# Optimization experiments

Measured on AMD Instinct MI355X. Metric: run time of the kernel, lower is better.

The kernel has to match this reference:

```python
import jax, jax.numpy as jnp
import numpy as np

E = 8        # numExperts
D = 1024     # d_model
F = 4096     # expert hidden = 4*d_model
T = 8192     # total tokens (sum of expertFrequency)


def setup_inputs() -> dict:
    key = jax.random.key(0)
    k0, k1, k2, k3, k4 = jax.random.split(key, 5)
    expertOrderedInput = jax.random.normal(k0, (T, D), dtype=jnp.float32)
    # Static equal split so the split sizes are jit-compatible.
    expertFrequency = jnp.full((E,), T // E, dtype=jnp.int64)
    s1 = 1.0 / np.sqrt(D)
    s2 = 1.0 / np.sqrt(F)
    w1 = jax.random.normal(k1, (E, D, F), dtype=jnp.float32) * s1
    b1 = jnp.zeros((E, F), dtype=jnp.float32)
    w2 = jax.random.normal(k2, (E, F, D), dtype=jnp.float32) * s2
    b2 = jnp.zeros((E, D), dtype=jnp.float32)
    return {"expertOrderedInput": expertOrderedInput,
            "expertFrequency": expertFrequency,
            "w1": w1, "b1": b1, "w2": w2, "b2": b2}


def reference(expertOrderedInput, expertFrequency, w1, b1, w2, b2):
    # expertOrderedInput: [T, D], tokens pre-sorted by expert.
    # expertFrequency is equal per expert (T/E each), so the
    # split-loop-cat in the torch module is exactly a grouped GEMM.
    e = w1.shape[0]
    t = expertOrderedInput.shape[0]
    x = expertOrderedInput.reshape(e, t // e, -1)            # [E, T/E, D]
    h = jax.nn.gelu(jnp.einsum('etd,edf->etf', x, w1) + b1[:, None, :])
    y = jnp.einsum('etf,efd->etd', h, w2) + b2[:, None, :]   # [E, T/E, D]
    return y.reshape(t, -1)                                   # cat along dim 0
```

## Files before the change

kernel.cpp:

```cpp
#include <hip/hip_runtime.h>

#define E_ 8
#define D_ 1024
#define F_ 4096
#define T_ 8192

typedef unsigned short u16;
typedef short bf16x8 __attribute__((ext_vector_type(8)));
typedef float f32x4 __attribute__((ext_vector_type(4)));
typedef unsigned short u16x8 __attribute__((ext_vector_type(8)));

__device__ __forceinline__ u16 f2bf(float f) {
    unsigned u = __builtin_bit_cast(unsigned, f);
    u += 0x7fffu + ((u >> 16) & 1u);
    return (u16)(u >> 16);
}

__device__ __forceinline__ float gelu_tanh(float x) {
    const float k0 = 0.7978845608028654f;
    const float k1 = 0.044715f;
    float t = tanhf(k0 * (x + k1 * x * x * x));
    return 0.5f * x * (1.0f + t);
}

__device__ __forceinline__ void async16(const void* g, void* l) {
    __builtin_amdgcn_global_load_lds(
        (const __attribute__((address_space(1))) unsigned int*)g,
        (__attribute__((address_space(3))) unsigned int*)l, 16, 0, 0);
}

__global__ void cvt_x(const float* __restrict__ in, u16* __restrict__ out) {
    int i = blockIdx.x * 256 + threadIdx.x;
    const float4* in4 = (const float4*)in;
    float4 a = in4[2 * i], b = in4[2 * i + 1];
    u16x8 o;
    o[0] = f2bf(a.x); o[1] = f2bf(a.y); o[2] = f2bf(a.z); o[3] = f2bf(a.w);
    o[4] = f2bf(b.x); o[5] = f2bf(b.y); o[6] = f2bf(b.z); o[7] = f2bf(b.w);
    *(u16x8*)(out + (size_t)i * 8) = o;
}

__global__ void transpose_cvt(const float* __restrict__ src, u16* __restrict__ dst,
                              int R, int C) {
    __shared__ float tile[32][33];
    int e = blockIdx.z;
    src += (size_t)e * R * C;
    dst += (size_t)e * R * C;
    int c0 = blockIdx.x * 32, r0 = blockIdx.y * 32;
    int tx = threadIdx.x, ty = threadIdx.y;
#pragma unroll
    for (int i = 0; i < 4; ++i)
        tile[ty + i * 8][tx] = src[(size_t)(r0 + ty + i * 8) * C + c0 + tx];
    __syncthreads();
#pragma unroll
    for (int i = 0; i < 4; ++i)
        dst[(size_t)(c0 + ty + i * 8) * R + r0 + tx] = f2bf(tile[tx][ty + i * 8]);
}

template <int BN, int WM, int WN, int EPI, int NM, int NN>
__global__ __launch_bounds__(512, 2) void gemm8p(
    const u16* __restrict__ A,
    const u16* __restrict__ Bt,
    const float* __restrict__ bias,
    void* __restrict__ Cv,
    int Mpe, int N, int K) {
    constexpr int BM  = 256;
    constexpr int LA  = 2;
    constexpr int LB  = BN / 128;
    constexpr int WTM = BM / WM;
    constexpr int MFR = WTM / 16;
    constexpr int AELEM = 4 * BM * 32;
    constexpr int VMC = 2 * (LA + LB);
    __shared__ u16 lds[AELEM + 4 * BN * 32];

    const int tid = threadIdx.x;
    const int w = tid >> 6, lane = tid & 63;
    const int lr = lane & 15, lg = lane >> 4;
    const int wm = w / WN, wn = w % WN;

    constexpr int NWG = E_ * NM * NN;
    constexpr int PER = NWG / 8;
    const int bid = blockIdx.x;
    const int logical = (bid & 7) * PER + (bid >> 3);
    const int e   = logical / (NM * NN);
    const int rem = logical % (NM * NN);
    const int bn  = rem / NM;
    const int bm  = rem % NM;

    A    += (size_t)e * Mpe * K;
    Bt   += (size_t)e * N * K;
    bias += (size_t)e * N;
    const int n0 = bn * BN;
    const int m0 = bm * BM;
    const int NT = K >> 6;

    const char* gA[LA];
    const char* gB[LB];
    {
        int kch = (lane & 3) ^ ((lane >> 3) & 3);
#pragma unroll
        for (int i = 0; i < LA; ++i) {
            int row = i * 128 + w * 16 + (lane >> 2);
            gA[i] = (const char*)(A + (size_t)(m0 + row) * K + kch * 8);
        }
#pragma unroll
        for (int i = 0; i < LB; ++i) {
            int row = i * 128 + w * 16 + (lane >> 2);
            gB[i] = (const char*)(Bt + (size_t)(n0 + row) * K + kch * 8);
        }
    }
    char* ldsc = (char*)lds;

    auto stageA = [&](int t, int h) {
        size_t goff = (size_t)t * 128 + (size_t)h * 64;
        unsigned dst = (unsigned)((((t & 1) * 2 + h) * (BM * 64)) + w * 1024);
#pragma unroll
        for (int i = 0; i < LA; ++i)
            async16(gA[i] + goff, ldsc + dst + i * 8192);
    };
    auto stageB = [&](int t, int h) {
        size_t goff = (size_t)t * 128 + (size_t)h * 64;
        unsigned dst = (unsigned)(AELEM * 2 + (((t & 1) * 2 + h) * (BN * 64)) + w * 1024);
#pragma unroll
        for (int i = 0; i < LB; ++i)
            async16(gB[i] + goff, ldsc + dst + i * 8192);
    };

    f32x4 acc[MFR][4];
    const f32x4 zero = {0.f, 0.f, 0.f, 0.f};
#pragma unroll
    for (int i = 0; i < MFR; ++i)
#pragma unroll
        for (int j = 0; j < 4; ++j) acc[i][j] = zero;

    stageA(0, 0); stageB(0, 0); stageA(0, 1); stageB(0, 1);
    stageA(1, 0); stageB(1, 0);
    asm volatile("s_waitcnt vmcnt(%0)" :: "i"(VMC) : "memory");
    __builtin_amdgcn_s_barrier();
    __builtin_amdgcn_sched_barrier(0);

    const u16* SBbase = lds + AELEM;
    bf16x8 a[MFR];
    const int arow = wm * WTM + lr;
    const int brow = wn * 64 + lr;
    const int axor = (lg ^ ((arow >> 1) & 3)) * 8;
    const int bxor = (lg ^ ((brow >> 1) & 3)) * 8;

    for (int c = 0; c < NT; ++c) {
        const int bb = c & 1;
        const u16* SA0 = lds    + (bb * 2 + 0) * (BM * 32);
        const u16* SA1 = lds    + (bb * 2 + 1) * (BM * 32);
        const u16* SB0 = SBbase + (bb * 2 + 0) * (BN * 32);
        const u16* SB1 = SBbase + (bb * 2 + 1) * (BN * 32);
        const bool stg1 = (c + 1 < NT);
        const bool stg2 = (c + 2 < NT);
        const bool tail = (c >= NT - 2);

#pragma unroll
        for (int i = 0; i < MFR; ++i)
            a[i] = *(const bf16x8*)(SA0 + (arow + i * 16) * 32 + axor);
        bf16x8 b0 = *(const bf16x8*)(SB0 + (brow +  0) * 32 + bxor);
        bf16x8 b1 = *(const bf16x8*)(SB0 + (brow + 16) * 32 + bxor);
        if (stg1) stageA(c + 1, 1);
        __builtin_amdgcn_s_barrier();
        __builtin_amdgcn_s_setprio(1);
#pragma unroll
        for (int i = 0; i < MFR; ++i) {
            acc[i][0] = __builtin_amdgcn_mfma_f32_16x16x32_bf16(a[i], b0, acc[i][0], 0, 0, 0);
            acc[i][1] = __builtin_amdgcn_mfma_f32_16x16x32_bf16(a[i], b1, acc[i][1], 0, 0, 0);
        }
        __builtin_amdgcn_s_setprio(0);
        __builtin_amdgcn_s_barrier();
        __builtin_amdgcn_sched_barrier(0);

        b0 = *(const bf16x8*)(SB0 + (brow + 32) * 32 + bxor);
        b1 = *(const bf16x8*)(SB0 + (brow + 48) * 32 + bxor);
        if (stg1) stageB(c + 1, 1);
        __builtin_amdgcn_s_barrier();
        __builtin_amdgcn_s_setprio(1);
#pragma unroll
        for (int i = 0; i < MFR; ++i) {
            acc[i][2] = __builtin_amdgcn_mfma_f32_16x16x32_bf16(a[i], b0, acc[i][2], 0, 0, 0);
            acc[i][3] = __builtin_amdgcn_mfma_f32_16x16x32_bf16(a[i], b1, acc[i][3], 0, 0, 0);
        }
        __builtin_amdgcn_s_setprio(0);
        if (tail) asm volatile("s_waitcnt vmcnt(0)" ::: "memory");
        else      asm volatile("s_waitcnt vmcnt(%0)" :: "i"(VMC) : "memory");
        __builtin_amdgcn_s_barrier();
        __builtin_amdgcn_sched_barrier(0);

#pragma unroll
        for (int i = 0; i < MFR; ++i)
            a[i] = *(const bf16x8*)(SA1 + (arow + i * 16) * 32 + axor);
        b0 = *(const bf16x8*)(SB1 + (brow +  0) * 32 + bxor);
        b1 = *(const bf16x8*)(SB1 + (brow + 16) * 32 + bxor);
        if (stg2) stageA(c + 2, 0);
        __builtin_amdgcn_s_barrier();
        __builtin_amdgcn_s_setprio(1);
#pragma unroll
        for (int i = 0; i < MFR; ++i) {
            acc[i][0] = __builtin_amdgcn_mfma_f32_16x16x32_bf16(a[i], b0, acc[i][0], 0, 0, 0);
            acc[i][1] = __builtin_amdgcn_mfma_f32_16x16x32_bf16(a[i], b1, acc[i][1], 0, 0, 0);
        }
        __builtin_amdgcn_s_setprio(0);
        __builtin_amdgcn_s_barrier();
        __builtin_amdgcn_sched_barrier(0);

        b0 = *(const bf16x8*)(SB1 + (brow + 32) * 32 + bxor);
        b1 = *(const bf16x8*)(SB1 + (brow + 48) * 32 + bxor);
        if (stg2) stageB(c + 2, 0);
        __builtin_amdgcn_s_barrier();
        __builtin_amdgcn_s_setprio(1);
#pragma unroll
        for (int i = 0; i < MFR; ++i) {
            acc[i][2] = __builtin_amdgcn_mfma_f32_16x16x32_bf16(a[i], b0, acc[i][2], 0, 0, 0);
            acc[i][3] = __builtin_amdgcn_mfma_f32_16x16x32_bf16(a[i], b1, acc[i][3], 0, 0, 0);
        }
        __builtin_amdgcn_s_setprio(0);
        if (tail) asm volatile("s_waitcnt vmcnt(0)" ::: "memory");
        else      asm volatile("s_waitcnt vmcnt(%0)" :: "i"(VMC) : "memory");
        __builtin_amdgcn_s_barrier();
        __builtin_amdgcn_sched_barrier(0);
    }

    const int mb = m0 + wm * WTM, nb = n0 + wn * 64;
    if constexpr (EPI == 1) {
        u16* C = (u16*)Cv + (size_t)e * Mpe * N;
#pragma unroll
        for (int i = 0; i < MFR; ++i) {
#pragma unroll
            for (int j = 0; j < 4; ++j) {
                int col = nb + j * 16 + lr;
                float bv = bias[col];
                int row = mb + i * 16 + lg * 4;
#pragma unroll
                for (int t = 0; t < 4; ++t) {
                    float v = acc[i][j][t] + bv;
                    C[(size_t)(row + t) * N + col] = f2bf(gelu_tanh(v));
                }
            }
        }
    } else {
        float* C = (float*)Cv + (size_t)e * Mpe * N;
#pragma unroll
        for (int i = 0; i < MFR; ++i) {
#pragma unroll
            for (int j = 0; j < 4; ++j) {
                int col = nb + j * 16 + lr;
                float bv = bias[col];
                int row = mb + i * 16 + lg * 4;
#pragma unroll
                for (int t = 0; t < 4; ++t)
                    C[(size_t)(row + t) * N + col] = acc[i][j][t] + bv;
            }
        }
    }
}

extern "C" void kernel_launch(void* const* d_in, const int* in_sizes, int n_in,
                              void* d_out, int out_size, void* d_ws, size_t ws_size,
                              hipStream_t stream) {
    const float* X  = (const float*)d_in[0];
    const float* w1 = (const float*)d_in[2];
    const float* b1 = (const float*)d_in[3];
    const float* w2 = (const float*)d_in[4];
    const float* b2 = (const float*)d_in[5];
    float* out = (float*)d_out;

    const size_t XBF_B = (size_t)T_ * D_ * 2;
    const size_t WT_B  = (size_t)E_ * F_ * D_ * 2;
    const size_t H_B   = (size_t)T_ * F_ * 2;
    if (ws_size < XBF_B + WT_B + H_B) return;

    char* ws = (char*)d_ws;
    u16* Xbf = (u16*)ws;
    u16* Wt  = (u16*)(ws + XBF_B);
    u16* H   = (u16*)(ws + XBF_B + WT_B);

    cvt_x<<<dim3((T_ * D_) / 8 / 256), dim3(256), 0, stream>>>(X, Xbf);
    transpose_cvt<<<dim3(F_ / 32, D_ / 32, E_), dim3(32, 8), 0, stream>>>(w1, Wt, D_, F_);
    gemm8p<256, 2, 4, 1, 4, 16><<<dim3(512), dim3(512), 0, stream>>>(
        Xbf, Wt, b1, H, T_ / E_, F_, D_);
    transpose_cvt<<<dim3(D_ / 32, F_ / 32, E_), dim3(32, 8), 0, stream>>>(w2, Wt, F_, D_);
    gemm8p<128, 4, 2, 0, 4, 8><<<dim3(256), dim3(512), 0, stream>>>(
        H, Wt, b2, out, T_ / E_, D_, F_);
}
```

Before: 269.1 us.

## Speed up GELU, widen weight transpose tiles, and tighten GEMM phase sync

Replaces the tanhf-based GELU with an equivalent exp2/rcp sigmoid form, x*sigmoid(2z), in the first GEMM epilogue. The weight transpose-convert kernel now uses 32x128 tiles and writes two bf16 values per store, which should give fewer blocks and wider writes. In the GEMM main loop it adds an explicit lgkmcnt(0) wait plus sched_barriers around each MFMA phase and unrolls the loop by 2. The fast reciprocal slightly changes GELU numerics, and the extra LDS wait could serialize some overlap.

```diff
diff --git a/kernel.cpp b/kernel.cpp
--- a/kernel.cpp
+++ b/kernel.cpp
@@ -9,6 +9,7 @@
 typedef short bf16x8 __attribute__((ext_vector_type(8)));
 typedef float f32x4 __attribute__((ext_vector_type(4)));
 typedef unsigned short u16x8 __attribute__((ext_vector_type(8)));
+typedef unsigned short u16x2 __attribute__((ext_vector_type(2)));
 
 __device__ __forceinline__ u16 f2bf(float f) {
     unsigned u = __builtin_bit_cast(unsigned, f);
@@ -16,11 +17,13 @@
     return (u16)(u >> 16);
 }
 
-__device__ __forceinline__ float gelu_tanh(float x) {
-    const float k0 = 0.7978845608028654f;
-    const float k1 = 0.044715f;
-    float t = tanhf(k0 * (x + k1 * x * x * x));
-    return 0.5f * x * (1.0f + t);
+__device__ __forceinline__ float gelu_fast(float x) {
+    const float a = -2.885390082f * 0.7978845608028654f;
+    const float b = a * 0.044715f;
+    float u = x * x;
+    float p = x * __builtin_fmaf(b, u, a);
+    float e = exp2f(p);
+    return x * __builtin_amdgcn_rcpf(1.0f + e);
 }
 
 __device__ __forceinline__ void async16(const void* g, void* l) {
@@ -39,21 +42,30 @@
     *(u16x8*)(out + (size_t)i * 8) = o;
 }
 
-__global__ void transpose_cvt(const float* __restrict__ src, u16* __restrict__ dst,
-                              int R, int C) {
-    __shared__ float tile[32][33];
+__global__ __launch_bounds__(256) void transpose_cvt(
+    const float* __restrict__ src, u16* __restrict__ dst, int R, int C) {
+    __shared__ float tile[32][129];
     int e = blockIdx.z;
     src += (size_t)e * R * C;
     dst += (size_t)e * R * C;
-    int c0 = blockIdx.x * 32, r0 = blockIdx.y * 32;
-    int tx = threadIdx.x, ty = threadIdx.y;
-#pragma unroll
-    for (int i = 0; i < 4; ++i)
-        tile[ty + i * 8][tx] = src[(size_t)(r0 + ty + i * 8) * C + c0 + tx];
+    int c0 = blockIdx.x * 32, r0 = blockIdx.y * 128;
+    int tid = threadIdx.x;
+    int lc = tid & 31, lr0 = tid >> 5;
+#pragma unroll
+    for (int i = 0; i < 16; ++i) {
+        int r = lr0 + i * 8;
+        tile[lc][r] = src[(size_t)(r0 + r) * C + c0 + lc];
+    }
     __syncthreads();
-#pragma unroll
-    for (int i = 0; i < 4; ++i)
-        dst[(size_t)(c0 + ty + i * 8) * R + r0 + tx] = f2bf(tile[tx][ty + i * 8]);
+    int sc = tid >> 6, sr = (tid & 63) * 2;
+#pragma unroll
+    for (int i = 0; i < 8; ++i) {
+        int c = sc + i * 4;
+        u16x2 v;
+        v[0] = f2bf(tile[c][sr]);
+        v[1] = f2bf(tile[c][sr + 1]);
+        *(u16x2*)(dst + (size_t)(c0 + c) * R + r0 + sr) = v;
+    }
 }
 
 template <int BN, int WM, int WN, int EPI, int NM, int NN>
@@ -145,6 +157,26 @@
     const int axor = (lg ^ ((arow >> 1) & 3)) * 8;
     const int bxor = (lg ^ ((brow >> 1) & 3)) * 8;
 
+#define PH_OPEN()                                          \
+    __builtin_amdgcn_sched_barrier(0);                     \
+    __builtin_amdgcn_s_barrier();                          \
+    asm volatile("s_waitcnt lgkmcnt(0)" ::: "memory");     \
+    __builtin_amdgcn_sched_barrier(0);                     \
+    __builtin_amdgcn_s_setprio(1);
+#define PH_CLOSE()                                         \
+    __builtin_amdgcn_s_setprio(0);                         \
+    __builtin_amdgcn_sched_barrier(0);                     \
+    __builtin_amdgcn_s_barrier();                          \
+    __builtin_amdgcn_sched_barrier(0);
+#define PH_CLOSE_VM()                                      \
+    __builtin_amdgcn_s_setprio(0);                         \
+    __builtin_amdgcn_sched_barrier(0);                     \
+    if (tail) asm volatile("s_waitcnt vmcnt(0)" ::: "memory");                \
+    else      asm volatile("s_waitcnt vmcnt(%0)" :: "i"(VMC) : "memory");     \
+    __builtin_amdgcn_s_barrier();                          \
+    __builtin_amdgcn_sched_barrier(0);
+
+#pragma unroll 2
     for (int c = 0; c < NT; ++c) {
         const int bb = c & 1;
         const u16* SA0 = lds    + (bb * 2 + 0) * (BM * 32);
@@ -161,32 +193,24 @@
         bf16x8 b0 = *(const bf16x8*)(SB0 + (brow +  0) * 32 + bxor);
         bf16x8 b1 = *(const bf16x8*)(SB0 + (brow + 16) * 32 + bxor);
         if (stg1) stageA(c + 1, 1);
-        __builtin_amdgcn_s_barrier();
-        __builtin_amdgcn_s_setprio(1);
+        PH_OPEN();
 #pragma unroll
         for (int i = 0; i < MFR; ++i) {
             acc[i][0] = __builtin_amdgcn_mfma_f32_16x16x32_bf16(a[i], b0, acc[i][0], 0, 0, 0);
             acc[i][1] = __builtin_amdgcn_mfma_f32_16x16x32_bf16(a[i], b1, acc[i][1], 0, 0, 0);
         }
-        __builtin_amdgcn_s_setprio(0);
-        __builtin_amdgcn_s_barrier();
-        __builtin_amdgcn_sched_barrier(0);
+        PH_CLOSE();
 
         b0 = *(const bf16x8*)(SB0 + (brow + 32) * 32 + bxor);
         b1 = *(const bf16x8*)(SB0 + (brow + 48) * 32 + bxor);
         if (stg1) stageB(c + 1, 1);
-        __builtin_amdgcn_s_barrier();
-        __builtin_amdgcn_s_setprio(1);
+        PH_OPEN();
 #pragma unroll
         for (int i = 0; i < MFR; ++i) {
             acc[i][2] = __builtin_amdgcn_mfma_f32_16x16x32_bf16(a[i], b0, acc[i][2], 0, 0, 0);
             acc[i][3] = __builtin_amdgcn_mfma_f32_16x16x32_bf16(a[i], b1, acc[i][3], 0, 0, 0);
         }
-        __builtin_amdgcn_s_setprio(0);
-        if (tail) asm volatile("s_waitcnt vmcnt(0)" ::: "memory");
-        else      asm volatile("s_waitcnt vmcnt(%0)" :: "i"(VMC) : "memory");
-        __builtin_amdgcn_s_barrier();
-        __builtin_amdgcn_sched_barrier(0);
+        PH_CLOSE_VM();
 
 #pragma unroll
         for (int i = 0; i < MFR; ++i)
@@ -194,33 +218,28 @@
         b0 = *(const bf16x8*)(SB1 + (brow +  0) * 32 + bxor);
         b1 = *(const bf16x8*)(SB1 + (brow + 16) * 32 + bxor);
         if (stg2) stageA(c + 2, 0);
-        __builtin_amdgcn_s_barrier();
-        __builtin_amdgcn_s_setprio(1);
+        PH_OPEN();
 #pragma unroll
         for (int i = 0; i < MFR; ++i) {
             acc[i][0] = __builtin_amdgcn_mfma_f32_16x16x32_bf16(a[i], b0, acc[i][0], 0, 0, 0);
             acc[i][1] = __builtin_amdgcn_mfma_f32_16x16x32_bf16(a[i], b1, acc[i][1], 0, 0, 0);
         }
-        __builtin_amdgcn_s_setprio(0);
-        __builtin_amdgcn_s_barrier();
-        __builtin_amdgcn_sched_barrier(0);
+        PH_CLOSE();
 
         b0 = *(const bf16x8*)(SB1 + (brow + 32) * 32 + bxor);
         b1 = *(const bf16x8*)(SB1 + (brow + 48) * 32 + bxor);
         if (stg2) stageB(c + 2, 0);
-        __builtin_amdgcn_s_barrier();
-        __builtin_amdgcn_s_setprio(1);
+        PH_OPEN();
 #pragma unroll
         for (int i = 0; i < MFR; ++i) {
             acc[i][2] = __builtin_amdgcn_mfma_f32_16x16x32_bf16(a[i], b0, acc[i][2], 0, 0, 0);
             acc[i][3] = __builtin_amdgcn_mfma_f32_16x16x32_bf16(a[i], b1, acc[i][3], 0, 0, 0);
         }
-        __builtin_amdgcn_s_setprio(0);
-        if (tail) asm volatile("s_waitcnt vmcnt(0)" ::: "memory");
-        else      asm volatile("s_waitcnt vmcnt(%0)" :: "i"(VMC) : "memory");
-        __builtin_amdgcn_s_barrier();
-        __builtin_amdgcn_sched_barrier(0);
-    }
+        PH_CLOSE_VM();
+    }
+#undef PH_OPEN
+#undef PH_CLOSE
+#undef PH_CLOSE_VM
 
     const int mb = m0 + wm * WTM, nb = n0 + wn * 64;
     if constexpr (EPI == 1) {
@@ -235,7 +254,7 @@
 #pragma unroll
                 for (int t = 0; t < 4; ++t) {
                     float v = acc[i][j][t] + bv;
-                    C[(size_t)(row + t) * N + col] = f2bf(gelu_tanh(v));
+                    C[(size_t)(row + t) * N + col] = f2bf(gelu_fast(v));
                 }
             }
         }
@@ -277,10 +296,10 @@
     u16* H   = (u16*)(ws + XBF_B + WT_B);
 
     cvt_x<<<dim3((T_ * D_) / 8 / 256), dim3(256), 0, stream>>>(X, Xbf);
-    transpose_cvt<<<dim3(F_ / 32, D_ / 32, E_), dim3(32, 8), 0, stream>>>(w1, Wt, D_, F_);
+    transpose_cvt<<<dim3(F_ / 32, D_ / 128, E_), dim3(256), 0, stream>>>(w1, Wt, D_, F_);
     gemm8p<256, 2, 4, 1, 4, 16><<<dim3(512), dim3(512), 0, stream>>>(
         Xbf, Wt, b1, H, T_ / E_, F_, D_);
-    transpose_cvt<<<dim3(D_ / 32, F_ / 32, E_), dim3(32, 8), 0, stream>>>(w2, Wt, F_, D_);
+    transpose_cvt<<<dim3(D_ / 32, F_ / 128, E_), dim3(256), 0, stream>>>(w2, Wt, F_, D_);
     gemm8p<128, 4, 2, 0, 4, 8><<<dim3(256), dim3(512), 0, stream>>>(
         H, Wt, b2, out, T_ / E_, D_, F_);
 }
```

New measurement: 250.7 us. -6.8%, faster.
